# Performance work log

Hardware: AMD Instinct MI355X
Metric: run time of the kernel (lower is better)

The kernel has to match this reference:

```python
import jax, jax.numpy as jnp
import numpy as np

N_NODES = 100000
N_EDGES = 1600000
N_GRAPHS = 1024
IN_FEATS = 74
HID = 100


def setup_inputs() -> dict:
    key = jax.random.key(0)
    ks = jax.random.split(key, 16)
    node_feats = jax.random.normal(ks[0], (N_NODES, IN_FEATS), dtype=jnp.float32)
    src = jax.random.randint(ks[1], (N_EDGES,), 0, N_NODES, dtype=jnp.int32)
    dst = jax.random.randint(ks[2], (N_EDGES,), 0, N_NODES, dtype=jnp.int32)
    graph_ids = jnp.sort(jax.random.randint(ks[3], (N_NODES,), 0, N_GRAPHS, dtype=jnp.int32))

    def lin(k, fi, fo):
        s = 1.0 / np.sqrt(fi)
        kw, kb = jax.random.split(k)
        return (jax.random.uniform(kw, (fi, fo), jnp.float32, -s, s),
                jax.random.uniform(kb, (fo,), jnp.float32, -s, s))

    W_self1, _ = lin(ks[4], IN_FEATS, HID)
    W_neigh1, b1 = lin(ks[5], IN_FEATS, HID)
    W_self2, _ = lin(ks[6], HID, HID)
    W_neigh2, b2 = lin(ks[7], HID, HID)
    w_atom, b_atom = lin(ks[8], HID, 1)
    W_p1, b_p1 = lin(ks[9], 2 * HID, 64)
    W_p2, b_p2 = lin(ks[10], 64, 1)
    return {
        'node_feats': node_feats, 'src': src, 'dst': dst, 'graph_ids': graph_ids,
        'n_graphs': N_GRAPHS,
        'W_self1': W_self1, 'W_neigh1': W_neigh1, 'b1': b1,
        'W_self2': W_self2, 'W_neigh2': W_neigh2, 'b2': b2,
        'w_atom': w_atom, 'b_atom': b_atom,
        'W_p1': W_p1, 'b_p1': b_p1, 'W_p2': W_p2, 'b_p2': b_p2,
    }


def _sage_mean_layer(h, src, dst, W_self, W_neigh, b):
    # DGL SAGEConv, aggregator 'mean': out = h @ W_self + mean_{u->v}(h_u) @ W_neigh + b
    n = h.shape[0]
    msg = h[src]  # [E, F] gather
    agg = jax.ops.segment_sum(msg, dst, num_segments=n)
    deg = jax.ops.segment_sum(jnp.ones((src.shape[0],), h.dtype), dst, num_segments=n)
    h_neigh = agg / jnp.maximum(deg, 1.0)[:, None]
    return jax.nn.relu(h @ W_self + h_neigh @ W_neigh + b)


def reference(node_feats, src, dst, graph_ids, n_graphs,
              W_self1, W_neigh1, b1, W_self2, W_neigh2, b2,
              w_atom, b_atom, W_p1, b_p1, W_p2, b_p2):
    h = _sage_mean_layer(node_feats, src, dst, W_self1, W_neigh1, b1)
    h = _sage_mean_layer(h, src, dst, W_self2, W_neigh2, b2)

    # WeightedSumAndMax readout
    w = jax.nn.sigmoid(h @ w_atom + b_atom)          # [N, 1]
    g_sum = jax.ops.segment_sum(h * w, graph_ids, num_segments=n_graphs)   # [G, HID]
    g_max = jax.ops.segment_max(h, graph_ids, num_segments=n_graphs)       # [G, HID]
    g_max = jnp.where(jnp.isneginf(g_max), 0.0, g_max)  # empty graphs -> 0
    g_feats = jnp.concatenate([g_sum, g_max], axis=-1)  # [G, 2*HID]

    # MLP predictor: Linear(200,64) -> Linear(64,1) (no activation between)
    out = (g_feats @ W_p1 + b_p1) @ W_p2 + b_p2
    return out
```

## Files before the change

### kernel.cpp

```cpp
#include <hip/hip_runtime.h>

#define N_NODES 100000
#define N_PAD   100096
#define N_EDGES 1600000
#define N_GRAPHS 1024
#define F_IN 74
#define HID 100

#define KP1 160
#define KP2 224

#define FBF_LD 80
#define F8T_LD 80
#define AGT_LD 80
#define H1C8_LD 128
#define H2_LD  100

#define ZROW N_NODES

#define NB ((N_NODES + 255) / 256)
#define BKCAP 8192
#define BIN_EPB 4096
#define NBB ((N_EDGES + BIN_EPB - 1) / BIN_EPB)

typedef __attribute__((ext_vector_type(8))) short short8;
typedef __attribute__((ext_vector_type(4))) float f32x4;
typedef __attribute__((ext_vector_type(2))) float f32x2;

#if defined(__has_builtin)
#if __has_builtin(__builtin_amdgcn_cvt_pk_f32_fp8) && __has_builtin(__builtin_amdgcn_cvt_pk_fp8_f32)
#define HAVE_FP8 1
#endif
#endif

__device__ __forceinline__ unsigned short f2bf(float x) {
    union { float f; unsigned u; } c; c.f = x;
    unsigned u = c.u;
    unsigned r = (u + 0x7fffu + ((u >> 16) & 1u)) >> 16;
    return (unsigned short)r;
}
__device__ __forceinline__ float bf2f(unsigned short h) {
    union { unsigned u; float f; } c; c.u = ((unsigned)h) << 16;
    return c.f;
}
__device__ __forceinline__ float blo(unsigned w) { return bf2f((unsigned short)(w & 0xffffu)); }
__device__ __forceinline__ float bhi(unsigned w) { return bf2f((unsigned short)(w >> 16)); }
__device__ __forceinline__ unsigned bpack(float a, float b) {
    return (unsigned)f2bf(a) | ((unsigned)f2bf(b) << 16);
}
__device__ __forceinline__ void store8(void* p, unsigned lo, unsigned hi) {
    unsigned long long v = (unsigned long long)lo | ((unsigned long long)hi << 32);
    *(unsigned long long*)p = v;
}

__device__ __forceinline__ unsigned char enc_fp8_1(float v) {
#ifdef HAVE_FP8
    return (unsigned char)__builtin_amdgcn_cvt_pk_fp8_f32(v, 0.f, 0, false);
#else
    unsigned sgn = v < 0.f ? 0x80u : 0u;
    float m = fabsf(v);
    unsigned char mag;
    if (m < 0.015625f) {
        int q = (int)(m * 512.0f + 0.5f);
        mag = (unsigned char)(q > 7 ? 7 : q);
    } else {
        union { float f; unsigned u; } c; c.f = m;
        unsigned r = c.u + 0x7ffff + ((c.u >> 20) & 1u);
        int e = (int)(r >> 23) - 127;
        mag = (e > 8) ? (unsigned char)0x7e : (unsigned char)(((e + 7) << 3) | ((r >> 20) & 7u));
    }
    return (unsigned char)(sgn | mag);
#endif
}
__device__ __forceinline__ unsigned enc_fp8x4(float v0, float v1, float v2, float v3) {
#ifdef HAVE_FP8
    int r = __builtin_amdgcn_cvt_pk_fp8_f32(v0, v1, 0, false);
    r = __builtin_amdgcn_cvt_pk_fp8_f32(v2, v3, r, true);
    return (unsigned)r;
#else
    return (unsigned)enc_fp8_1(v0) | ((unsigned)enc_fp8_1(v1) << 8) |
           ((unsigned)enc_fp8_1(v2) << 16) | ((unsigned)enc_fp8_1(v3) << 24);
#endif
}
__device__ __forceinline__ void dec_fp8x4(unsigned w, float& x0, float& x1, float& x2, float& x3) {
#ifdef HAVE_FP8
    f32x2 lo = __builtin_amdgcn_cvt_pk_f32_fp8((int)w, false);
    f32x2 hi = __builtin_amdgcn_cvt_pk_f32_fp8((int)w, true);
    x0 = lo.x; x1 = lo.y; x2 = hi.x; x3 = hi.y;
#else
    auto d1 = [](unsigned b) -> float {
        float s = (b & 0x80u) ? -1.f : 1.f;
        b &= 0x7fu;
        if (b < 8) return s * (float)b * 0.001953125f;
        union { unsigned u; float f; } c;
        c.u = ((((b >> 3) & 15u) - 7 + 127) << 23) | ((b & 7u) << 20);
        return s * c.f;
    };
    x0 = d1(w & 0xffu); x1 = d1((w >> 8) & 0xffu);
    x2 = d1((w >> 16) & 0xffu); x3 = d1(w >> 24);
#endif
}


__global__ __launch_bounds__(256) void k_bin(const int* __restrict__ src,
                                             const int* __restrict__ dst,
                                             int* __restrict__ bucket_fill,
                                             unsigned* __restrict__ bbuf) {
    __shared__ int cnt[NB];
    __shared__ int base[NB];
    int t = threadIdx.x;
    for (int i = t; i < NB; i += 256) cnt[i] = 0;
    __syncthreads();
    int e0 = blockIdx.x * BIN_EPB;
    int e1 = e0 + BIN_EPB < N_EDGES ? e0 + BIN_EPB : N_EDGES;
    for (int e = e0 + t; e < e1; e += 256) {
        atomicAdd(&cnt[dst[e] >> 8], 1);
    }
    __syncthreads();
    for (int i = t; i < NB; i += 256) {
        int c = cnt[i];
        base[i] = c ? atomicAdd(&bucket_fill[i], c) : 0;
        cnt[i] = 0;
    }
    __syncthreads();
    for (int e = e0 + t; e < e1; e += 256) {
        int d = dst[e];
        int b = d >> 8;
        int pos = atomicAdd(&cnt[b], 1);
        bbuf[(size_t)b * BKCAP + base[b] + pos] = ((unsigned)src[e] << 8) | (unsigned)(d & 255);
    }
}


__global__ __launch_bounds__(256) void k_scatter(const unsigned* __restrict__ bbuf,
                                                 const int* __restrict__ bucket_fill,
                                                 int2* __restrict__ rp2,
                                                 int* __restrict__ csr) {
    __shared__ int fc[256];
    __shared__ int ofs[256];
    __shared__ int wsum[4];
    int b = blockIdx.x, t = threadIdx.x;
    int nstart = b << 8;
    int base = b * BKCAP;
    int bend = base + bucket_fill[b];
    fc[t] = 0;
    __syncthreads();
    for (int i = base + t; i < bend; i += 256)
        atomicAdd(&fc[bbuf[i] & 255u], 1);
    __syncthreads();
    int d = fc[t];
    int dp = (d + 7) & ~7;
    int lane = t & 63, w = t >> 6;
    int inc = dp;
    #pragma unroll
    for (int o = 1; o < 64; o <<= 1) {
        int x = __shfl_up(inc, o, 64);
        if (lane >= o) inc += x;
    }
    if (lane == 63) wsum[w] = inc;
    __syncthreads();
    int woff = 0;
    for (int i = 0; i < w; ++i) woff += wsum[i];
    ofs[t] = base + woff + inc - dp;
    __syncthreads();
    int node = nstart + t;
    int o0 = ofs[t];
    if (node < N_NODES) rp2[node] = make_int2(o0, o0 + d);
    for (int i = o0 + d; i < o0 + dp; ++i) csr[i] = ZROW;
    fc[t] = 0;
    __syncthreads();
    for (int i = base + t; i < bend; i += 256) {
        unsigned p = bbuf[i];
        int dl = (int)(p & 255u);
        int pos = atomicAdd(&fc[dl], 1);
        csr[ofs[dl] + pos] = (int)(p >> 8);
    }
}


__global__ void k_feats(const float* __restrict__ feats, short* __restrict__ fbf,
                        unsigned* __restrict__ f8t, unsigned* __restrict__ h1c8) {
    int idx = blockIdx.x * blockDim.x + threadIdx.x;
    if (idx < H1C8_LD / 4) h1c8[(size_t)ZROW * (H1C8_LD / 4) + idx] = 0u;
    if (idx >= (N_NODES + 1) * (F8T_LD / 4)) return;
    int n = idx / (F8T_LD / 4), g = idx - n * (F8T_LD / 4);
    int c0 = 4 * g;
    float v0 = 0.f, v1 = 0.f, v2 = 0.f, v3 = 0.f;
    if (n < N_NODES) {
        const float* r = feats + (size_t)n * F_IN;
        v0 = (c0 + 0 < F_IN) ? r[c0 + 0] : 0.f;
        v1 = (c0 + 1 < F_IN) ? r[c0 + 1] : 0.f;
        v2 = (c0 + 2 < F_IN) ? r[c0 + 2] : 0.f;
        v3 = (c0 + 3 < F_IN) ? r[c0 + 3] : 0.f;
    }
    unsigned* fb = (unsigned*)fbf + (size_t)n * (FBF_LD / 2) + 2 * g;
    fb[0] = bpack(v0, v1);
    fb[1] = bpack(v2, v3);
    f8t[idx] = enc_fp8x4(v0, v1, v2, v3);
}


template <int KP, int K1, int AGG0>
__global__ void k_wconv(const float* __restrict__ Ws, const float* __restrict__ Wn,
                        short* __restrict__ Whi, short* __restrict__ Wlo) {
    int idx = blockIdx.x * blockDim.x + threadIdx.x;
    if (idx >= 112 * KP) return;
    int col = idx / KP, k = idx - col * KP;
    float v = 0.f;
    if (col < HID) {
        if (k < K1) v = Ws[k * HID + col];
        else if (k >= AGG0 && k < AGG0 + K1) v = Wn[(k - AGG0) * HID + col];
    }
    unsigned short hi = f2bf(v);
    unsigned short lo = f2bf(v - bf2f(hi));
    Whi[idx] = (short)hi;
    Wlo[idx] = (short)lo;
}


__global__ __launch_bounds__(256) void k_prep1(const unsigned char* __restrict__ f8t,
                        const int2* __restrict__ rp2, const int* __restrict__ csr,
                        short* __restrict__ agt) {
    int wid = threadIdx.x >> 6, lane = threadIdx.x & 63;
    int v = blockIdx.x * 4 + wid;
    if (v >= N_NODES) return;
    int h = lane >> 5, q = lane & 31;
    int2 se = rp2[v];
    int s = se.x, e = se.y;
    int deg = e - s;
    int pe = s + ((deg + 7) & ~7);
    float a0 = 0.f, a1 = 0.f, a2 = 0.f, a3 = 0.f;
    if (q < 19) {
        #pragma unroll 2
        for (int j = s; j < pe; j += 8) {
            unsigned w0 = *(const unsigned*)(f8t + (size_t)csr[j + h] * F8T_LD + q * 4);
            unsigned w1 = *(const unsigned*)(f8t + (size_t)csr[j + 2 + h] * F8T_LD + q * 4);
            unsigned w2 = *(const unsigned*)(f8t + (size_t)csr[j + 4 + h] * F8T_LD + q * 4);
            unsigned w3 = *(const unsigned*)(f8t + (size_t)csr[j + 6 + h] * F8T_LD + q * 4);
            float x0, x1, x2, x3;
            dec_fp8x4(w0, x0, x1, x2, x3); a0 += x0; a1 += x1; a2 += x2; a3 += x3;
            dec_fp8x4(w1, x0, x1, x2, x3); a0 += x0; a1 += x1; a2 += x2; a3 += x3;
            dec_fp8x4(w2, x0, x1, x2, x3); a0 += x0; a1 += x1; a2 += x2; a3 += x3;
            dec_fp8x4(w3, x0, x1, x2, x3); a0 += x0; a1 += x1; a2 += x2; a3 += x3;
        }
    }
    a0 += __shfl_xor(a0, 32, 64);
    a1 += __shfl_xor(a1, 32, 64);
    a2 += __shfl_xor(a2, 32, 64);
    a3 += __shfl_xor(a3, 32, 64);
    float inv = 1.0f / fmaxf((float)deg, 1.0f);
    if (h == 0 && q < 20) {
        store8((char*)agt + (size_t)v * (AGT_LD * 2) + q * 8,
               bpack(a0 * inv, a1 * inv), bpack(a2 * inv, a3 * inv));
    }
}


__global__ __launch_bounds__(256) void k_prep2(const unsigned char* __restrict__ h1c8,
                        const int2* __restrict__ rp2, const int* __restrict__ csr,
                        short* __restrict__ X2) {
    int wid = threadIdx.x >> 6, lane = threadIdx.x & 63;
    int v = blockIdx.x * 4 + wid;
    if (v >= N_NODES) return;
    int h = lane >> 5, q = lane & 31;
    int2 se = rp2[v];
    int s = se.x, e = se.y;
    int deg = e - s;
    int pe = s + ((deg + 7) & ~7);
    float a0 = 0.f, a1 = 0.f, a2 = 0.f, a3 = 0.f;
    if (q < 25) {
        #pragma unroll 2
        for (int j = s; j < pe; j += 8) {
            unsigned w0 = *(const unsigned*)(h1c8 + (size_t)csr[j + h] * H1C8_LD + q * 4);
            unsigned w1 = *(const unsigned*)(h1c8 + (size_t)csr[j + 2 + h] * H1C8_LD + q * 4);
            unsigned w2 = *(const unsigned*)(h1c8 + (size_t)csr[j + 4 + h] * H1C8_LD + q * 4);
            unsigned w3 = *(const unsigned*)(h1c8 + (size_t)csr[j + 6 + h] * H1C8_LD + q * 4);
            float x0, x1, x2, x3;
            dec_fp8x4(w0, x0, x1, x2, x3); a0 += x0; a1 += x1; a2 += x2; a3 += x3;
            dec_fp8x4(w1, x0, x1, x2, x3); a0 += x0; a1 += x1; a2 += x2; a3 += x3;
            dec_fp8x4(w2, x0, x1, x2, x3); a0 += x0; a1 += x1; a2 += x2; a3 += x3;
            dec_fp8x4(w3, x0, x1, x2, x3); a0 += x0; a1 += x1; a2 += x2; a3 += x3;
        }
    }
    a0 += __shfl_xor(a0, 32, 64);
    a1 += __shfl_xor(a1, 32, 64);
    a2 += __shfl_xor(a2, 32, 64);
    a3 += __shfl_xor(a3, 32, 64);
    float inv = 1.0f / fmaxf((float)deg, 1.0f);
    char* Xw = (char*)X2 + (size_t)v * (KP2 * 2);
    if (h == 0 && q < 25) {
        store8(Xw + 200 + q * 8, bpack(a0 * inv, a1 * inv), bpack(a2 * inv, a3 * inv));
    }
    if (h == 1 && q < 6) {
        store8(Xw + 400 + q * 8, 0u, 0u);
    }
}


__global__ __launch_bounds__(256) void k_mfma1(
    const short* __restrict__ fbf, const short* __restrict__ agt,
    const short* __restrict__ Wthi, const short* __restrict__ Wtlo,
    const float* __restrict__ bias,
    short* __restrict__ X2, unsigned char* __restrict__ h1c8) {
    int t = threadIdx.x;
    int wid = t >> 6, lane = t & 63;
    int quad = lane >> 4, lr = lane & 15;
    int rowbase = blockIdx.x * 128 + wid * 32;

    f32x4 acc[2][7];
    #pragma unroll
    for (int rf = 0; rf < 2; ++rf)
        #pragma unroll
        for (int n = 0; n < 7; ++n) acc[rf][n] = (f32x4){0.f, 0.f, 0.f, 0.f};

    #pragma unroll
    for (int c = 0; c < 5; ++c) {
        short8 ah[2], wh[7], wl[7];
        #pragma unroll
        for (int rf = 0; rf < 2; ++rf) {
            int row = rowbase + rf * 16 + lr;
            const short* p;
            if (c < 2) p = fbf + (size_t)row * FBF_LD + c * 32 + quad * 8;
            else if (c == 2) p = (quad < 2) ? fbf + (size_t)row * FBF_LD + 64 + quad * 8
                                            : agt + (size_t)row * AGT_LD + (quad - 2) * 8;
            else p = agt + (size_t)row * AGT_LD + (c - 3) * 32 + 16 + quad * 8;
            ah[rf] = *(const short8*)p;
        }
        #pragma unroll
        for (int n = 0; n < 7; ++n) {
            size_t off = (size_t)(n * 16 + lr) * KP1 + c * 32 + quad * 8;
            wh[n] = *(const short8*)(Wthi + off);
            wl[n] = *(const short8*)(Wtlo + off);
        }
        #pragma unroll
        for (int rf = 0; rf < 2; ++rf)
            #pragma unroll
            for (int n = 0; n < 7; ++n) {
                acc[rf][n] = __builtin_amdgcn_mfma_f32_16x16x32_bf16(ah[rf], wh[n], acc[rf][n], 0, 0, 0);
                acc[rf][n] = __builtin_amdgcn_mfma_f32_16x16x32_bf16(ah[rf], wl[n], acc[rf][n], 0, 0, 0);
            }
    }

    #pragma unroll
    for (int rf = 0; rf < 2; ++rf) {
        #pragma unroll
        for (int n = 0; n < 7; ++n) {
            int col = n * 16 + lr;
            if (col < HID) {
                float bv = bias[col];
                #pragma unroll
                for (int r = 0; r < 4; ++r) {
                    int row = rowbase + rf * 16 + quad * 4 + r;
                    if (row < N_NODES) {
                        float v = fmaxf(acc[rf][n][r] + bv, 0.f);
                        X2[(size_t)row * KP2 + col] = (short)f2bf(v);
                        h1c8[(size_t)row * H1C8_LD + col] = enc_fp8_1(v);
                    }
                }
            }
        }
    }
}


__global__ __launch_bounds__(256) void k_mfma2(
    const short* __restrict__ X2,
    const short* __restrict__ Wthi, const short* __restrict__ Wtlo,
    const float* __restrict__ bias, short* __restrict__ h2c) {
    int t = threadIdx.x;
    int wid = t >> 6, lane = t & 63;
    int quad = lane >> 4, lr = lane & 15;
    int rowbase = blockIdx.x * 128 + wid * 32;

    f32x4 acc[2][7];
    #pragma unroll
    for (int rf = 0; rf < 2; ++rf)
        #pragma unroll
        for (int n = 0; n < 7; ++n) acc[rf][n] = (f32x4){0.f, 0.f, 0.f, 0.f};

    #pragma unroll
    for (int c = 0; c < 7; ++c) {
        short8 ah[2], wh[7], wl[7];
        #pragma unroll
        for (int rf = 0; rf < 2; ++rf) {
            size_t off = (size_t)(rowbase + rf * 16 + lr) * KP2 + c * 32 + quad * 8;
            ah[rf] = *(const short8*)(X2 + off);
        }
        #pragma unroll
        for (int n = 0; n < 7; ++n) {
            size_t off = (size_t)(n * 16 + lr) * KP2 + c * 32 + quad * 8;
            wh[n] = *(const short8*)(Wthi + off);
            wl[n] = *(const short8*)(Wtlo + off);
        }
        #pragma unroll
        for (int rf = 0; rf < 2; ++rf)
            #pragma unroll
            for (int n = 0; n < 7; ++n) {
                acc[rf][n] = __builtin_amdgcn_mfma_f32_16x16x32_bf16(ah[rf], wh[n], acc[rf][n], 0, 0, 0);
                acc[rf][n] = __builtin_amdgcn_mfma_f32_16x16x32_bf16(ah[rf], wl[n], acc[rf][n], 0, 0, 0);
            }
    }

    #pragma unroll
    for (int rf = 0; rf < 2; ++rf) {
        #pragma unroll
        for (int n = 0; n < 7; ++n) {
            int col = n * 16 + lr;
            if (col < HID) {
                float bv = bias[col];
                #pragma unroll
                for (int r = 0; r < 4; ++r) {
                    int row = rowbase + rf * 16 + quad * 4 + r;
                    if (row < N_NODES) {
                        float v = fmaxf(acc[rf][n][r] + bv, 0.f);
                        h2c[(size_t)row * H2_LD + col] = (short)f2bf(v);
                    }
                }
            }
        }
    }
}


__global__ void k_weff(const float* __restrict__ Wp1, const float* __restrict__ bp1,
                       const float* __restrict__ Wp2, const float* __restrict__ bp2,
                       float* __restrict__ weff) {
    int t = threadIdx.x;
    if (t < 200) {
        float s = 0.f;
        for (int k = 0; k < 64; ++k) s += Wp1[t * 64 + k] * Wp2[k];
        weff[t] = s;
    } else if (t == 200) {
        float s = bp2[0];
        for (int k = 0; k < 64; ++k) s += bp1[k] * Wp2[k];
        weff[200] = s;
    }
}


__global__ __launch_bounds__(128) void k_readout(
    const unsigned short* __restrict__ h2c, const int* __restrict__ graph_ids,
    const float* __restrict__ w_atom, const float* __restrict__ b_atom,
    const float* __restrict__ weff, float* __restrict__ out) {
    int g = blockIdx.x;
    int t = threadIdx.x, lane = t & 63, w = t >> 6;

    int s_, e_;
    {
        int l = 0, r = N_NODES;
        while (l < r) { int m = (l + r) >> 1; if (graph_ids[m] < g) l = m + 1; else r = m; }
        s_ = l;
        l = s_; r = N_NODES;
        while (l < r) { int m = (l + r) >> 1; if (graph_ids[m] < g + 1) l = m + 1; else r = m; }
        e_ = l;
    }

    float ba = b_atom[0];
    float wa0 = 0.f, wa1 = 0.f;
    if (lane < 50) {
        float2 wv = *(const float2*)&w_atom[2 * lane];
        wa0 = wv.x; wa1 = wv.y;
    }
    float sum0 = 0.f, sum1 = 0.f, mx0 = 0.f, mx1 = 0.f;
    for (int i = s_ + w; i < e_; i += 2) {
        float v0 = 0.f, v1 = 0.f;
        if (lane < 50) {
            unsigned wv = *(const unsigned*)(h2c + (size_t)i * H2_LD + 2 * lane);
            v0 = blo(wv); v1 = bhi(wv);
        }
        float p = v0 * wa0 + v1 * wa1;
        #pragma unroll
        for (int off = 32; off; off >>= 1) p += __shfl_xor(p, off, 64);
        float wt = 1.f / (1.f + __expf(-(p + ba)));
        sum0 += v0 * wt;
        sum1 += v1 * wt;
        mx0 = fmaxf(mx0, v0);
        mx1 = fmaxf(mx1, v1);
    }

    __shared__ float ssum[2][HID];
    __shared__ float smx[2][HID];
    if (lane < 50) {
        ssum[w][2 * lane] = sum0;
        ssum[w][2 * lane + 1] = sum1;
        smx[w][2 * lane] = mx0;
        smx[w][2 * lane + 1] = mx1;
    }
    __syncthreads();

    float contrib = 0.f;
    if (t < HID) {
        float sumf = ssum[0][t] + ssum[1][t];
        float mxf = fmaxf(smx[0][t], smx[1][t]);
        contrib = sumf * weff[t] + mxf * weff[HID + t];
    }
    #pragma unroll
    for (int off = 32; off; off >>= 1) contrib += __shfl_xor(contrib, off, 64);
    __shared__ float red[2];
    if (lane == 0) red[w] = contrib;
    __syncthreads();
    if (t == 0) out[g] = red[0] + red[1] + weff[200];
}


extern "C" void kernel_launch(void* const* d_in, const int* in_sizes, int n_in,
                              void* d_out, int out_size, void* d_ws, size_t ws_size,
                              hipStream_t stream) {
    const float* node_feats = (const float*)d_in[0];
    const int* src = (const int*)d_in[1];
    const int* dst = (const int*)d_in[2];
    const int* gid = (const int*)d_in[3];
    const float* Ws1 = (const float*)d_in[5];
    const float* Wn1 = (const float*)d_in[6];
    const float* b1 = (const float*)d_in[7];
    const float* Ws2 = (const float*)d_in[8];
    const float* Wn2 = (const float*)d_in[9];
    const float* b2 = (const float*)d_in[10];
    const float* w_atom = (const float*)d_in[11];
    const float* b_atom = (const float*)d_in[12];
    const float* Wp1 = (const float*)d_in[13];
    const float* bp1 = (const float*)d_in[14];
    const float* Wp2 = (const float*)d_in[15];
    const float* bp2 = (const float*)d_in[16];
    float* out = (float*)d_out;

    char* ws = (char*)d_ws;
    size_t off = 0;
    auto alloc = [&](size_t bytes) -> void* {
        void* p = (void*)(ws + off);
        off += (bytes + 255) & ~(size_t)255;
        return p;
    };
    int2* rp2 = (int2*)alloc((size_t)N_NODES * sizeof(int2));
    int* bucket_fill = (int*)alloc(NB * sizeof(int));
    int* csr = (int*)alloc((size_t)NB * BKCAP * sizeof(int));
    unsigned* bbuf = (unsigned*)alloc((size_t)NB * BKCAP * sizeof(unsigned));
    short* fbf = (short*)alloc((size_t)(N_PAD + 1) * FBF_LD * sizeof(short));
    unsigned char* f8t = (unsigned char*)alloc((size_t)(N_PAD + 1) * F8T_LD);
    short* agt = (short*)alloc((size_t)N_PAD * AGT_LD * sizeof(short));
    short* X2 = (short*)alloc((size_t)N_PAD * KP2 * sizeof(short));
    unsigned char* h1c8 = (unsigned char*)alloc((size_t)(N_NODES + 1) * H1C8_LD);
    short* h2c = (short*)alloc((size_t)N_NODES * H2_LD * sizeof(short));
    short* Wt1hi = (short*)alloc(112 * KP1 * sizeof(short));
    short* Wt1lo = (short*)alloc(112 * KP1 * sizeof(short));
    short* Wt2hi = (short*)alloc(112 * KP2 * sizeof(short));
    short* Wt2lo = (short*)alloc(112 * KP2 * sizeof(short));
    float* weff = (float*)alloc(256 * sizeof(float));

    hipMemsetAsync(bucket_fill, 0, NB * sizeof(int), stream);

    k_bin<<<NBB, 256, 0, stream>>>(src, dst, bucket_fill, bbuf);
    k_scatter<<<NB, 256, 0, stream>>>(bbuf, bucket_fill, rp2, csr);

    k_feats<<<((N_NODES + 1) * (F8T_LD / 4) + 255) / 256, 256, 0, stream>>>(
        node_feats, fbf, (unsigned*)f8t, (unsigned*)h1c8);
    k_wconv<KP1, F_IN, 80><<<(112 * KP1 + 255) / 256, 256, 0, stream>>>(Ws1, Wn1, Wt1hi, Wt1lo);
    k_wconv<KP2, HID, 100><<<(112 * KP2 + 255) / 256, 256, 0, stream>>>(Ws2, Wn2, Wt2hi, Wt2lo);

    k_prep1<<<(N_NODES + 3) / 4, 256, 0, stream>>>(f8t, rp2, csr, agt);
    k_mfma1<<<N_PAD / 128, 256, 0, stream>>>(fbf, agt, Wt1hi, Wt1lo, b1, X2, h1c8);
    k_prep2<<<(N_NODES + 3) / 4, 256, 0, stream>>>(h1c8, rp2, csr, X2);
    k_mfma2<<<N_PAD / 128, 256, 0, stream>>>(X2, Wt2hi, Wt2lo, b2, h2c);

    k_weff<<<1, 256, 0, stream>>>(Wp1, bp1, Wp2, bp2, weff);
    k_readout<<<N_GRAPHS, 128, 0, stream>>>((const unsigned short*)h2c, gid, w_atom, b_atom, weff, out);
}
```

Measured before the change: 262.0 us.

## Halve MFMA row tile per wave and split atom weights out of readout

Both MFMA GEMM kernels now give each wave 16 rows instead of 32, which doubles the grid and cuts accumulator registers. This should raise occupancy, but each block reloads the weight fragments over half as many rows. The readout's per-node sigmoid attention weight moves into a new fully parallel kernel (k_atomw) that writes a per-node buffer. Readout then uses 4 waves per graph and needs no per-node shuffle reduction. The cost is one extra launch and an extra pass over h2c.

```diff
diff --git a/kernel.cpp b/kernel.cpp
--- a/kernel.cpp
+++ b/kernel.cpp
@@ -130,7 +130,6 @@
         bbuf[(size_t)b * BKCAP + base[b] + pos] = ((unsigned)src[e] << 8) | (unsigned)(d & 255);
     }
 }
-
 
 __global__ __launch_bounds__(256) void k_scatter(const unsigned* __restrict__ bbuf,
                                                  const int* __restrict__ bucket_fill,
@@ -305,26 +304,23 @@
     int t = threadIdx.x;
     int wid = t >> 6, lane = t & 63;
     int quad = lane >> 4, lr = lane & 15;
-    int rowbase = blockIdx.x * 128 + wid * 32;
-
-    f32x4 acc[2][7];
-    #pragma unroll
-    for (int rf = 0; rf < 2; ++rf)
-        #pragma unroll
-        for (int n = 0; n < 7; ++n) acc[rf][n] = (f32x4){0.f, 0.f, 0.f, 0.f};
+    int rowbase = blockIdx.x * 64 + wid * 16;
+
+    f32x4 acc[7];
+    #pragma unroll
+    for (int n = 0; n < 7; ++n) acc[n] = (f32x4){0.f, 0.f, 0.f, 0.f};
 
     #pragma unroll
     for (int c = 0; c < 5; ++c) {
-        short8 ah[2], wh[7], wl[7];
-        #pragma unroll
-        for (int rf = 0; rf < 2; ++rf) {
-            int row = rowbase + rf * 16 + lr;
+        short8 ah, wh[7], wl[7];
+        {
+            int row = rowbase + lr;
             const short* p;
             if (c < 2) p = fbf + (size_t)row * FBF_LD + c * 32 + quad * 8;
             else if (c == 2) p = (quad < 2) ? fbf + (size_t)row * FBF_LD + 64 + quad * 8
                                             : agt + (size_t)row * AGT_LD + (quad - 2) * 8;
             else p = agt + (size_t)row * AGT_LD + (c - 3) * 32 + 16 + quad * 8;
-            ah[rf] = *(const short8*)p;
+            ah = *(const short8*)p;
         }
         #pragma unroll
         for (int n = 0; n < 7; ++n) {
@@ -333,29 +329,24 @@
             wl[n] = *(const short8*)(Wtlo + off);
         }
         #pragma unroll
-        for (int rf = 0; rf < 2; ++rf)
+        for (int n = 0; n < 7; ++n) {
+            acc[n] = __builtin_amdgcn_mfma_f32_16x16x32_bf16(ah, wh[n], acc[n], 0, 0, 0);
+            acc[n] = __builtin_amdgcn_mfma_f32_16x16x32_bf16(ah, wl[n], acc[n], 0, 0, 0);
+        }
+    }
+
+    #pragma unroll
+    for (int n = 0; n < 7; ++n) {
+        int col = n * 16 + lr;
+        if (col < HID) {
+            float bv = bias[col];
             #pragma unroll
-            for (int n = 0; n < 7; ++n) {
-                acc[rf][n] = __builtin_amdgcn_mfma_f32_16x16x32_bf16(ah[rf], wh[n], acc[rf][n], 0, 0, 0);
-                acc[rf][n] = __builtin_amdgcn_mfma_f32_16x16x32_bf16(ah[rf], wl[n], acc[rf][n], 0, 0, 0);
-            }
-    }
-
-    #pragma unroll
-    for (int rf = 0; rf < 2; ++rf) {
-        #pragma unroll
-        for (int n = 0; n < 7; ++n) {
-            int col = n * 16 + lr;
-            if (col < HID) {
-                float bv = bias[col];
-                #pragma unroll
-                for (int r = 0; r < 4; ++r) {
-                    int row = rowbase + rf * 16 + quad * 4 + r;
-                    if (row < N_NODES) {
-                        float v = fmaxf(acc[rf][n][r] + bv, 0.f);
-                        X2[(size_t)row * KP2 + col] = (short)f2bf(v);
-                        h1c8[(size_t)row * H1C8_LD + col] = enc_fp8_1(v);
-                    }
+            for (int r = 0; r < 4; ++r) {
+                int row = rowbase + quad * 4 + r;
+                if (row < N_NODES) {
+                    float v = fmaxf(acc[n][r] + bv, 0.f);
+                    X2[(size_t)row * KP2 + col] = (short)f2bf(v);
+                    h1c8[(size_t)row * H1C8_LD + col] = enc_fp8_1(v);
                 }
             }
         }
@@ -370,21 +361,18 @@
     int t = threadIdx.x;
     int wid = t >> 6, lane = t & 63;
     int quad = lane >> 4, lr = lane & 15;
-    int rowbase = blockIdx.x * 128 + wid * 32;
-
-    f32x4 acc[2][7];
-    #pragma unroll
-    for (int rf = 0; rf < 2; ++rf)
-        #pragma unroll
-        for (int n = 0; n < 7; ++n) acc[rf][n] = (f32x4){0.f, 0.f, 0.f, 0.f};
+    int rowbase = blockIdx.x * 64 + wid * 16;
+
+    f32x4 acc[7];
+    #pragma unroll
+    for (int n = 0; n < 7; ++n) acc[n] = (f32x4){0.f, 0.f, 0.f, 0.f};
 
     #pragma unroll
     for (int c = 0; c < 7; ++c) {
-        short8 ah[2], wh[7], wl[7];
-        #pragma unroll
-        for (int rf = 0; rf < 2; ++rf) {
-            size_t off = (size_t)(rowbase + rf * 16 + lr) * KP2 + c * 32 + quad * 8;
-            ah[rf] = *(const short8*)(X2 + off);
+        short8 ah, wh[7], wl[7];
+        {
+            size_t off = (size_t)(rowbase + lr) * KP2 + c * 32 + quad * 8;
+            ah = *(const short8*)(X2 + off);
         }
         #pragma unroll
         for (int n = 0; n < 7; ++n) {
@@ -393,32 +381,46 @@
             wl[n] = *(const short8*)(Wtlo + off);
         }
         #pragma unroll
-        for (int rf = 0; rf < 2; ++rf)
+        for (int n = 0; n < 7; ++n) {
+            acc[n] = __builtin_amdgcn_mfma_f32_16x16x32_bf16(ah, wh[n], acc[n], 0, 0, 0);
+            acc[n] = __builtin_amdgcn_mfma_f32_16x16x32_bf16(ah, wl[n], acc[n], 0, 0, 0);
+        }
+    }
+
+    #pragma unroll
+    for (int n = 0; n < 7; ++n) {
+        int col = n * 16 + lr;
+        if (col < HID) {
+            float bv = bias[col];
             #pragma unroll
-            for (int n = 0; n < 7; ++n) {
-                acc[rf][n] = __builtin_amdgcn_mfma_f32_16x16x32_bf16(ah[rf], wh[n], acc[rf][n], 0, 0, 0);
-                acc[rf][n] = __builtin_amdgcn_mfma_f32_16x16x32_bf16(ah[rf], wl[n], acc[rf][n], 0, 0, 0);
-            }
-    }
-
-    #pragma unroll
-    for (int rf = 0; rf < 2; ++rf) {
-        #pragma unroll
-        for (int n = 0; n < 7; ++n) {
-            int col = n * 16 + lr;
-            if (col < HID) {
-                float bv = bias[col];
-                #pragma unroll
-                for (int r = 0; r < 4; ++r) {
-                    int row = rowbase + rf * 16 + quad * 4 + r;
-                    if (row < N_NODES) {
-                        float v = fmaxf(acc[rf][n][r] + bv, 0.f);
-                        h2c[(size_t)row * H2_LD + col] = (short)f2bf(v);
-                    }
+            for (int r = 0; r < 4; ++r) {
+                int row = rowbase + quad * 4 + r;
+                if (row < N_NODES) {
+                    float v = fmaxf(acc[n][r] + bv, 0.f);
+                    h2c[(size_t)row * H2_LD + col] = (short)f2bf(v);
                 }
             }
         }
     }
+}
+
+
+__global__ __launch_bounds__(256) void k_atomw(
+    const unsigned short* __restrict__ h2c, const float* __restrict__ w_atom,
+    const float* __restrict__ b_atom, float* __restrict__ aw) {
+    int t = threadIdx.x;
+    int hw = t >> 5, q = t & 31;
+    int row = blockIdx.x * 8 + hw;
+    if (row >= N_NODES) return;
+    float dot = 0.f;
+    if (q < 25) {
+        uint2 v = *(const uint2*)(h2c + (size_t)row * H2_LD + q * 4);
+        float4 wa = *(const float4*)&w_atom[q * 4];
+        dot = blo(v.x) * wa.x + bhi(v.x) * wa.y + blo(v.y) * wa.z + bhi(v.y) * wa.w;
+    }
+    #pragma unroll
+    for (int off = 16; off; off >>= 1) dot += __shfl_xor(dot, off, 32);
+    if (q == 0) aw[row] = 1.f / (1.f + __expf(-(dot + b_atom[0])));
 }
 
 
@@ -438,10 +440,10 @@
 }
 
 
-__global__ __launch_bounds__(128) void k_readout(
-    const unsigned short* __restrict__ h2c, const int* __restrict__ graph_ids,
-    const float* __restrict__ w_atom, const float* __restrict__ b_atom,
-    const float* __restrict__ weff, float* __restrict__ out) {
+__global__ __launch_bounds__(256) void k_readout(
+    const unsigned short* __restrict__ h2c, const float* __restrict__ aw,
+    const int* __restrict__ graph_ids, const float* __restrict__ weff,
+    float* __restrict__ out) {
     int g = blockIdx.x;
     int t = threadIdx.x, lane = t & 63, w = t >> 6;
 
@@ -455,31 +457,21 @@
         e_ = l;
     }
 
-    float ba = b_atom[0];
-    float wa0 = 0.f, wa1 = 0.f;
-    if (lane < 50) {
-        float2 wv = *(const float2*)&w_atom[2 * lane];
-        wa0 = wv.x; wa1 = wv.y;
-    }
     float sum0 = 0.f, sum1 = 0.f, mx0 = 0.f, mx1 = 0.f;
-    for (int i = s_ + w; i < e_; i += 2) {
-        float v0 = 0.f, v1 = 0.f;
+    for (int i = s_ + w; i < e_; i += 4) {
+        float wt = aw[i];
         if (lane < 50) {
             unsigned wv = *(const unsigned*)(h2c + (size_t)i * H2_LD + 2 * lane);
-            v0 = blo(wv); v1 = bhi(wv);
-        }
-        float p = v0 * wa0 + v1 * wa1;
-        #pragma unroll
-        for (int off = 32; off; off >>= 1) p += __shfl_xor(p, off, 64);
-        float wt = 1.f / (1.f + __expf(-(p + ba)));
-        sum0 += v0 * wt;
-        sum1 += v1 * wt;
-        mx0 = fmaxf(mx0, v0);
-        mx1 = fmaxf(mx1, v1);
-    }
-
-    __shared__ float ssum[2][HID];
-    __shared__ float smx[2][HID];
+            float v0 = blo(wv), v1 = bhi(wv);
+            sum0 += v0 * wt;
+            sum1 += v1 * wt;
+            mx0 = fmaxf(mx0, v0);
+            mx1 = fmaxf(mx1, v1);
+        }
+    }
+
+    __shared__ float ssum[4][HID];
+    __shared__ float smx[4][HID];
     if (lane < 50) {
         ssum[w][2 * lane] = sum0;
         ssum[w][2 * lane + 1] = sum1;
@@ -490,16 +482,16 @@
 
     float contrib = 0.f;
     if (t < HID) {
-        float sumf = ssum[0][t] + ssum[1][t];
-        float mxf = fmaxf(smx[0][t], smx[1][t]);
+        float sumf = ssum[0][t] + ssum[1][t] + ssum[2][t] + ssum[3][t];
+        float mxf = fmaxf(fmaxf(smx[0][t], smx[1][t]), fmaxf(smx[2][t], smx[3][t]));
         contrib = sumf * weff[t] + mxf * weff[HID + t];
     }
     #pragma unroll
     for (int off = 32; off; off >>= 1) contrib += __shfl_xor(contrib, off, 64);
-    __shared__ float red[2];
+    __shared__ float red[4];
     if (lane == 0) red[w] = contrib;
     __syncthreads();
-    if (t == 0) out[g] = red[0] + red[1] + weff[200];
+    if (t == 0) out[g] = red[0] + red[1] + red[2] + red[3] + weff[200];
 }
 
 
@@ -541,6 +533,7 @@
     short* X2 = (short*)alloc((size_t)N_PAD * KP2 * sizeof(short));
     unsigned char* h1c8 = (unsigned char*)alloc((size_t)(N_NODES + 1) * H1C8_LD);
     short* h2c = (short*)alloc((size_t)N_NODES * H2_LD * sizeof(short));
+    float* aw = (float*)alloc((size_t)N_NODES * sizeof(float));
     short* Wt1hi = (short*)alloc(112 * KP1 * sizeof(short));
     short* Wt1lo = (short*)alloc(112 * KP1 * sizeof(short));
     short* Wt2hi = (short*)alloc(112 * KP2 * sizeof(short));
@@ -558,10 +551,11 @@
     k_wconv<KP2, HID, 100><<<(112 * KP2 + 255) / 256, 256, 0, stream>>>(Ws2, Wn2, Wt2hi, Wt2lo);
 
     k_prep1<<<(N_NODES + 3) / 4, 256, 0, stream>>>(f8t, rp2, csr, agt);
-    k_mfma1<<<N_PAD / 128, 256, 0, stream>>>(fbf, agt, Wt1hi, Wt1lo, b1, X2, h1c8);
+    k_mfma1<<<N_PAD / 64, 256, 0, stream>>>(fbf, agt, Wt1hi, Wt1lo, b1, X2, h1c8);
     k_prep2<<<(N_NODES + 3) / 4, 256, 0, stream>>>(h1c8, rp2, csr, X2);
-    k_mfma2<<<N_PAD / 128, 256, 0, stream>>>(X2, Wt2hi, Wt2lo, b2, h2c);
-
+    k_mfma2<<<N_PAD / 64, 256, 0, stream>>>(X2, Wt2hi, Wt2lo, b2, h2c);
+
+    k_atomw<<<(N_NODES + 7) / 8, 256, 0, stream>>>((const unsigned short*)h2c, w_atom, b_atom, aw);
     k_weff<<<1, 256, 0, stream>>>(Wp1, bp1, Wp2, bp2, weff);
-    k_readout<<<N_GRAPHS, 128, 0, stream>>>((const unsigned short*)h2c, gid, w_atom, b_atom, weff, out);
-}
+    k_readout<<<N_GRAPHS, 256, 0, stream>>>((const unsigned short*)h2c, aw, gid, weff, out);
+}
```

After: 267.0 us. About the same (+1.9%).
